# Kernel optimization log

Measured on AMD Instinct MI355X. Metric: run time of the kernel, lower is better.

The kernel has to match this reference:

```python
import jax, jax.numpy as jnp
import numpy as np

B, RES, DIM, H, KD = 16, 32, 768, 12, 64
N = RES * RES          # 1024 tokens
D = KD                 # attn_ratio = 1 -> per-head value dim == key_dim
DH = D * H             # 768
SCALE = KD ** -0.5
LN_EPS = 1e-5


def _bias_idxs():
    # replicate the itertools.product construction: for row-major points,
    # offsets (|dy|,|dx|) are first seen in order dy-major, so id = |dy|*RES + |dx|
    coords = np.arange(N)
    y, x = coords // RES, coords % RES
    dy = np.abs(y[:, None] - y[None, :])
    dx = np.abs(x[:, None] - x[None, :])
    return jnp.asarray(dy * RES + dx, dtype=jnp.int32)  # [N, N]


def setup_inputs() -> dict:
    key = jax.random.key(0)
    ks = jax.random.split(key, 8)
    return {
        "x": jax.random.normal(ks[0], (B, N, DIM), jnp.float32),
        "ln_w": 1.0 + 0.01 * jax.random.normal(ks[1], (DIM,), jnp.float32),
        "ln_b": 0.01 * jax.random.normal(ks[2], (DIM,), jnp.float32),
        "qkv_w": 0.02 * jax.random.normal(ks[3], (3 * H * KD, DIM), jnp.float32),
        "qkv_b": 0.01 * jax.random.normal(ks[4], (3 * H * KD,), jnp.float32),
        "proj_w": 0.02 * jax.random.normal(ks[5], (DIM, DH), jnp.float32),
        "proj_b": 0.01 * jax.random.normal(ks[6], (DIM,), jnp.float32),
        "attn_biases": 0.1 * jax.random.normal(ks[7], (H, RES * RES), jnp.float32),
        "bias_idxs": _bias_idxs(),
    }


def reference(x, ln_w, ln_b, qkv_w, qkv_b, proj_w, proj_b, attn_biases, bias_idxs):
    # LayerNorm over the feature dim
    mu = jnp.mean(x, axis=-1, keepdims=True)
    var = jnp.mean(jnp.square(x - mu), axis=-1, keepdims=True)
    xn = (x - mu) * jax.lax.rsqrt(var + LN_EPS) * ln_w + ln_b

    # fused qkv projection -> [B, N, H, 3*KD], split per head
    qkv = (xn @ qkv_w.T + qkv_b).reshape(B, N, H, 3 * KD)
    q, k, v = jnp.split(qkv, [KD, 2 * KD], axis=3)  # each [B, N, H, KD]

    # gathered relative-position bias: [H, N, N]
    bias = attn_biases[:, bias_idxs]

    # scores + bias -> softmax -> AV
    attn = jnp.einsum("bnhk,bmhk->bhnm", q, k) * SCALE + bias[None]
    attn = jax.nn.softmax(attn, axis=-1)
    out = jnp.einsum("bhnm,bmhd->bnhd", attn, v).reshape(B, N, DH)
    return out @ proj_w.T + proj_b
```

## Files before the change

kernel.cpp:

```cpp
#include <hip/hip_runtime.h>
#include <cstdint>
#include <cstddef>

#define AS1 __attribute__((address_space(1)))
#define AS3 __attribute__((address_space(3)))

typedef float f32x4 __attribute__((ext_vector_type(4)));
typedef __bf16 bf16x8 __attribute__((ext_vector_type(8)));
typedef __bf16 bf16x4 __attribute__((ext_vector_type(4)));
typedef uint32_t u32x4 __attribute__((ext_vector_type(4)));

__device__ __forceinline__ void async_cp16(void* lds, const void* g) {
    __builtin_amdgcn_global_load_lds((AS1 void*)(g), (AS3 void*)(lds), 16, 0, 0);
}

__device__ __forceinline__ bf16x8 frag_of(u32x4 u) {
    return __builtin_bit_cast(bf16x8, u);
}

__global__ __launch_bounds__(256)
void cvt_w(const float* __restrict__ qkvw, const float* __restrict__ projw,
           __bf16* __restrict__ qkvwb, __bf16* __restrict__ projwb) {
    int i = blockIdx.x * 256 + threadIdx.x;
    if (i < 442368) {
        int row = i / 192, c4 = (i - row * 192) * 4;
        int t = (row >= 1536) ? 2 : (row >= 768 ? 1 : 0);
        int rem = row - t * 768;
        int hh = rem >> 6, d = rem & 63;
        int in_row = hh * 192 + t * 64 + d;
        float4 v = *(const float4*)(qkvw + (long)in_row * 768 + c4);
        bf16x4 o;
        o[0] = (__bf16)v.x; o[1] = (__bf16)v.y; o[2] = (__bf16)v.z; o[3] = (__bf16)v.w;
        *(bf16x4*)(qkvwb + (long)row * 768 + c4) = o;
    } else {
        int j = i - 442368;
        float4 v = ((const float4*)projw)[j];
        bf16x4 o;
        o[0] = (__bf16)v.x; o[1] = (__bf16)v.y; o[2] = (__bf16)v.z; o[3] = (__bf16)v.w;
        ((bf16x4*)projwb)[j] = o;
    }
}

__global__ __launch_bounds__(256)
void ln_kernel(const float* __restrict__ x, const float* __restrict__ w,
               const float* __restrict__ bsh, __bf16* __restrict__ xn) {
    const int lane = threadIdx.x & 63;
    const long row = (long)blockIdx.x * 4 + (threadIdx.x >> 6);
    const float4* xr = (const float4*)(x + row * 768);
    float4 v[3];
    v[0] = xr[lane]; v[1] = xr[lane + 64]; v[2] = xr[lane + 128];
    float s = 0.f, ss = 0.f;
#pragma unroll
    for (int i = 0; i < 3; ++i) {
        s  += v[i].x + v[i].y + v[i].z + v[i].w;
        ss += v[i].x * v[i].x + v[i].y * v[i].y + v[i].z * v[i].z + v[i].w * v[i].w;
    }
#pragma unroll
    for (int m = 1; m < 64; m <<= 1) { s += __shfl_xor(s, m); ss += __shfl_xor(ss, m); }
    const float mean = s * (1.f / 768.f);
    const float rstd = rsqrtf(ss * (1.f / 768.f) - mean * mean + 1e-5f);
    const float4* wv = (const float4*)w;
    const float4* bv = (const float4*)bsh;
    bf16x4* outp = (bf16x4*)(xn + row * 768);
#pragma unroll
    for (int i = 0; i < 3; ++i) {
        float4 wi = wv[lane + 64 * i], bi = bv[lane + 64 * i];
        bf16x4 o;
        o[0] = (__bf16)((v[i].x - mean) * rstd * wi.x + bi.x);
        o[1] = (__bf16)((v[i].y - mean) * rstd * wi.y + bi.y);
        o[2] = (__bf16)((v[i].z - mean) * rstd * wi.z + bi.z);
        o[3] = (__bf16)((v[i].w - mean) * rstd * wi.w + bi.w);
        outp[lane + 64 * i] = o;
    }
}

template <int MODE>
__device__ __forceinline__
void gemm_core(char* smem,
               const __bf16* __restrict__ A, const __bf16* __restrict__ Bw,
               const float* __restrict__ bias,
               __bf16* __restrict__ q_out, __bf16* __restrict__ k_out,
               __bf16* __restrict__ vt_out, float* __restrict__ f_out,
               long bm, long bn) {
    constexpr int K = 768;
    const int tid  = threadIdx.x;
    const int lane = tid & 63;
    const int quad = lane >> 4;
    const int l16  = lane & 15;
    const int wave = tid >> 6;
    const int wm = wave >> 1, wn = wave & 1;

    const __bf16* Ab = A  + bm * K;
    const __bf16* Bb = Bw + bn * K;

    const int e0 = tid, e1 = tid + 256;
    const int rA0 = e0 >> 2, c0 = ((e0 & 3) ^ ((e0 >> 3) & 3)) * 8;
    const int rA1 = e1 >> 2, c1 = ((e1 & 3) ^ ((e1 >> 3) & 3)) * 8;
    const int swq = quad ^ ((l16 >> 1) & 3);

    f32x4 acc[4][4] = {};

    auto stage = [&](int t) {
        char* base = smem + (t & 1) * 16384;
        const __bf16* As_ = Ab + t * 32;
        const __bf16* Bs_ = Bb + t * 32;
        async_cp16(base + e0 * 16,        As_ + (long)rA0 * K + c0);
        async_cp16(base + e1 * 16,        As_ + (long)rA1 * K + c1);
        async_cp16(base + 8192 + e0 * 16, Bs_ + (long)rA0 * K + c0);
        async_cp16(base + 8192 + e1 * 16, Bs_ + (long)rA1 * K + c1);
    };

    auto kstep = [&](int buf) {
        const u32x4* Av = (const u32x4*)(smem + buf * 16384);
        const u32x4* Bv = (const u32x4*)(smem + buf * 16384 + 8192);
        bf16x8 af[4], bfr[4];
#pragma unroll
        for (int t = 0; t < 4; ++t) {
            af[t]  = frag_of(Av[(wm * 64 + t * 16 + l16) * 4 + swq]);
            bfr[t] = frag_of(Bv[(wn * 64 + t * 16 + l16) * 4 + swq]);
        }
        __builtin_amdgcn_s_setprio(1);
#pragma unroll
        for (int i = 0; i < 4; ++i)
#pragma unroll
            for (int j = 0; j < 4; ++j) {
                if constexpr (MODE == 0)
                    acc[i][j] = __builtin_amdgcn_mfma_f32_16x16x32_bf16(bfr[j], af[i], acc[i][j], 0, 0, 0);
                else
                    acc[i][j] = __builtin_amdgcn_mfma_f32_16x16x32_bf16(af[i], bfr[j], acc[i][j], 0, 0, 0);
            }
        __builtin_amdgcn_s_setprio(0);
    };

    stage(0); stage(1);
    for (int t = 0; t < 24; ++t) {
        if (t < 23) { asm volatile("s_waitcnt vmcnt(4)" ::: "memory"); }
        else        { asm volatile("s_waitcnt vmcnt(0)" ::: "memory"); }
        __builtin_amdgcn_s_barrier();
        kstep(t & 1);
        asm volatile("s_waitcnt lgkmcnt(0)" ::: "memory");
        __builtin_amdgcn_s_barrier();
        if (t < 22) stage(t + 2);
    }

    if constexpr (MODE == 0) {
#pragma unroll
        for (int j = 0; j < 4; ++j) {
            int col0 = (int)bn + wn * 64 + j * 16 + quad * 4;
            int t  = col0 >= 768;
            int cc = col0 - t * 768;
            int h  = cc >> 6, d = cc & 63;
            int f  = h * 192 + t * 64 + d;
            float4 bb = *(const float4*)(bias + f);
            __bf16* dst = t ? k_out : q_out;
#pragma unroll
            for (int i = 0; i < 4; ++i) {
                long row = bm + wm * 64 + i * 16 + l16;
                long b   = row >> 10;
                long n   = row & 1023;
                bf16x4 pk;
                pk[0] = (__bf16)(acc[i][j][0] + bb.x);
                pk[1] = (__bf16)(acc[i][j][1] + bb.y);
                pk[2] = (__bf16)(acc[i][j][2] + bb.z);
                pk[3] = (__bf16)(acc[i][j][3] + bb.w);
                *(bf16x4*)(dst + ((b * 12 + h) * 1024 + n) * 64 + d) = pk;
            }
        }
    } else if constexpr (MODE == 2) {
#pragma unroll
        for (int j = 0; j < 4; ++j) {
            int cv = (int)bn - 1536 + wn * 64 + j * 16 + l16;
            int h  = cv >> 6, d = cv & 63;
            float bv = bias[h * 192 + 128 + d];
#pragma unroll
            for (int i = 0; i < 4; ++i) {
                long row0 = bm + wm * 64 + i * 16 + quad * 4;
                long b    = row0 >> 10;
                long n0   = row0 & 1023;
                bf16x4 pk;
                pk[0] = (__bf16)(acc[i][j][0] + bv);
                pk[1] = (__bf16)(acc[i][j][1] + bv);
                pk[2] = (__bf16)(acc[i][j][2] + bv);
                pk[3] = (__bf16)(acc[i][j][3] + bv);
                *(bf16x4*)(vt_out + ((b * 12 + h) * 64 + d) * 1024 + n0) = pk;
            }
        }
    } else {
#pragma unroll
        for (int i = 0; i < 4; ++i) {
#pragma unroll
            for (int r = 0; r < 4; ++r) {
                long row = bm + wm * 64 + i * 16 + quad * 4 + r;
#pragma unroll
                for (int j = 0; j < 4; ++j) {
                    int col = (int)bn + wn * 64 + j * 16 + l16;
                    f_out[row * 768 + col] = acc[i][j][r] + bias[col];
                }
            }
        }
    }
}

__global__ __launch_bounds__(256, 4)
void gemm_qkv(const __bf16* __restrict__ A, const __bf16* __restrict__ Bw,
              const float* __restrict__ bias, __bf16* __restrict__ qb,
              __bf16* __restrict__ kb, __bf16* __restrict__ vtb) {
    __shared__ __align__(16) char smem[32768];
    int blk  = blockIdx.x;
    int xcd  = blk & 7;
    int rest = blk >> 3;
    int bx   = rest % 18;
    int byg  = rest / 18;
    long by  = xcd + 8 * byg;
    if (bx < 12)
        gemm_core<0>(smem, A, Bw, bias, qb, kb, nullptr, nullptr, by * 128, (long)bx * 128);
    else
        gemm_core<2>(smem, A, Bw, bias, nullptr, nullptr, vtb, nullptr, by * 128, (long)bx * 128);
}

__global__ __launch_bounds__(256, 4)
void gemm_proj(const __bf16* __restrict__ A, const __bf16* __restrict__ Bw,
               const float* __restrict__ bias, float* __restrict__ out) {
    __shared__ __align__(16) char smem[32768];
    int blk  = blockIdx.x;
    int xcd  = blk & 7;
    int rest = blk >> 3;
    int bx   = rest % 6;
    int byg  = rest / 6;
    long by  = xcd + 8 * byg;
    gemm_core<1>(smem, A, Bw, bias, nullptr, nullptr, nullptr, out,
                 by * 128, (long)bx * 128);
}

__global__ __launch_bounds__(256, 4)
void attn_kernel(const __bf16* __restrict__ Q, const __bf16* __restrict__ Kb,
                 const __bf16* __restrict__ Vt, const float* __restrict__ biases,
                 __bf16* __restrict__ out) {
    __shared__ __align__(16) char smem[28672];
    float* brow = (float*)(smem + 24576);

    const int tid  = threadIdx.x;
    const int lane = tid & 63;
    const int wave = tid >> 6;
    const int quad = lane >> 4;
    const int l16  = lane & 15;
    const int sw   = l16 & 7;
    const int swp  = (l16 >> 1) & 3;

    int blk  = blockIdx.x;
    int xcd  = blk & 7;
    int rest = blk >> 3;
    int qt   = rest & 7;
    int bhg  = rest >> 3;
    int bh_i = xcd + 8 * bhg;
    int b    = bh_i / 12;
    int h    = bh_i - b * 12;

    const long bh = bh_i;
    const __bf16* Qg  = Q  + (bh * 1024 + qt * 128) * 64;
    const __bf16* Kg  = Kb + bh * 1024 * 64;
    const __bf16* Vtg = Vt + bh * 64 * 1024;

    const int rk = tid >> 3;
    const int ck = (tid & 7) ^ (rk & 7);
    const int rv = tid >> 2;
    const int cv = (tid & 3) ^ ((tid >> 3) & 3);

    {
        const float LOG2E = 1.4426950408889634f;
        float4 v = ((const float4*)(biases + (long)h * 1024))[tid];
        float4 o; o.x = v.x * LOG2E; o.y = v.y * LOG2E;
        o.z = v.z * LOG2E; o.w = v.w * LOG2E;
        ((float4*)brow)[tid] = o;
    }
#pragma unroll
    for (int j = 0; j < 4; ++j) {
        int e = tid + 256 * j;
        int r = e >> 3, c = (e & 7) ^ (r & 7);
        async_cp16(smem + e * 16, Qg + r * 64 + c * 8);
    }
    __syncthreads();

    bf16x8 aq[2][2];
    {
        const u32x4* Qv = (const u32x4*)smem;
#pragma unroll
        for (int g = 0; g < 2; ++g) {
            int qrow = wave * 32 + g * 16 + l16;
            aq[g][0] = frag_of(Qv[qrow * 8 + (quad ^ sw)]);
            aq[g][1] = frag_of(Qv[qrow * 8 + ((quad + 4) ^ sw)]);
        }
    }
    __syncthreads();
    async_cp16(smem + tid * 16,        Kg  + rk * 64   + ck * 8);
    async_cp16(smem + 8192 + tid * 16, Vtg + rv * 1024 + cv * 8);
    __syncthreads();

    const int yq = 4 * qt + wave;
    int pdx00[4], pdx01[4], pdx10[4];
#pragma unroll
    for (int r = 0; r < 4; ++r) {
        int d0 = l16 - (quad * 4 + r);
        pdx00[r] = d0 < 0 ? -d0 : d0;
        pdx01[r] = 16 - d0;
        pdx10[r] = 16 + d0;
    }

    const float SSCALE = 0.125f * 1.4426950408889634f;
    float lacc[2] = {0.f, 0.f};
    f32x4 o[2][4] = {};
    char* Pw = smem + 16384 + wave * 2048;
    const int hb = (quad & 1) * 8;
    const int pslotw = (quad >> 1);

    for (int kt = 0; kt < 32; ++kt) {
        const int cb = kt & 1;
        if (kt < 31) {
            const int nb = cb ^ 1;
            async_cp16(smem + nb * 4096 + tid * 16,
                       Kg + (kt + 1) * 2048 + rk * 64 + ck * 8);
            async_cp16(smem + 8192 + nb * 4096 + tid * 16,
                       Vtg + (kt + 1) * 32 + rv * 1024 + cv * 8);
        }

        f32x4 s[2][2];
        const u32x4* Kv = (const u32x4*)(smem + cb * 4096);
#pragma unroll
        for (int nt = 0; nt < 2; ++nt) {
            int krow = nt * 16 + l16;
            bf16x8 k0 = frag_of(Kv[krow * 8 + (quad ^ sw)]);
            bf16x8 k1 = frag_of(Kv[krow * 8 + ((quad + 4) ^ sw)]);
#pragma unroll
            for (int g = 0; g < 2; ++g) {
                f32x4 z = {0.f, 0.f, 0.f, 0.f};
                z = __builtin_amdgcn_mfma_f32_16x16x32_bf16(k0, aq[g][0], z, 0, 0, 0);
                z = __builtin_amdgcn_mfma_f32_16x16x32_bf16(k1, aq[g][1], z, 0, 0, 0);
                s[g][nt] = z;
            }
        }

        int dyv = yq - kt; dyv = dyv < 0 ? -dyv : dyv;
        const float* br = brow + dyv * 32;
#pragma unroll
        for (int g = 0; g < 2; ++g) {
#pragma unroll
            for (int nt = 0; nt < 2; ++nt) {
                const int* pdx = (g == nt) ? pdx00 : (g ? pdx10 : pdx01);
                bf16x4 pk;
#pragma unroll
                for (int r = 0; r < 4; ++r) {
                    float p = __builtin_amdgcn_exp2f(s[g][nt][r] * SSCALE + br[pdx[r]]);
                    lacc[g] += p;
                    pk[r] = (__bf16)p;
                }
                int slot = (nt * 2 + pslotw) ^ swp;
                *(bf16x4*)(Pw + (g * 16 + l16) * 64 + slot * 16 + hb) = pk;
            }
        }

        bf16x8 bp[2];
#pragma unroll
        for (int g = 0; g < 2; ++g)
            bp[g] = frag_of(*(const u32x4*)(Pw + (g * 16 + l16) * 64 + ((quad ^ swp) << 4)));
        const char* Vb = smem + 8192 + cb * 4096;
#pragma unroll
        for (int dt = 0; dt < 4; ++dt) {
            bf16x8 vf = frag_of(*(const u32x4*)(Vb + (dt * 16 + l16) * 64 + ((quad ^ swp) << 4)));
#pragma unroll
            for (int g = 0; g < 2; ++g)
                o[g][dt] = __builtin_amdgcn_mfma_f32_16x16x32_bf16(vf, bp[g], o[g][dt], 0, 0, 0);
        }

        __syncthreads();
    }

#pragma unroll
    for (int g = 0; g < 2; ++g) {
        float la = lacc[g];
        la += __shfl_xor(la, 16);
        la += __shfl_xor(la, 32);
        const float rl = 1.f / la;
        const long n = qt * 128 + wave * 32 + g * 16 + l16;
        __bf16* op = out + ((long)b * 1024 + n) * 768 + h * 64 + quad * 4;
#pragma unroll
        for (int dt = 0; dt < 4; ++dt) {
            bf16x4 ov;
            ov[0] = (__bf16)(o[g][dt][0] * rl);
            ov[1] = (__bf16)(o[g][dt][1] * rl);
            ov[2] = (__bf16)(o[g][dt][2] * rl);
            ov[3] = (__bf16)(o[g][dt][3] * rl);
            *(bf16x4*)(op + dt * 16) = ov;
        }
    }
}

extern "C" void kernel_launch(void* const* d_in, const int* in_sizes, int n_in,
                              void* d_out, int out_size, void* d_ws, size_t ws_size,
                              hipStream_t stream) {
    (void)in_sizes; (void)n_in; (void)out_size; (void)ws_size;
    const float* x      = (const float*)d_in[0];
    const float* ln_w   = (const float*)d_in[1];
    const float* ln_b   = (const float*)d_in[2];
    const float* qkv_w  = (const float*)d_in[3];
    const float* qkv_b  = (const float*)d_in[4];
    const float* proj_w = (const float*)d_in[5];
    const float* proj_b = (const float*)d_in[6];
    const float* ab     = (const float*)d_in[7];
    float* outp = (float*)d_out;

    char* ws = (char*)d_ws;
    __bf16* xn     = (__bf16*)(ws);
    __bf16* aout   = (__bf16*)(ws);
    __bf16* qkvwb  = (__bf16*)(ws + 25165824);
    __bf16* projwb = (__bf16*)(ws + 28704768);
    __bf16* qb     = (__bf16*)(ws + 29884416);
    __bf16* kb     = (__bf16*)(ws + 55050240);
    __bf16* vtb    = (__bf16*)(ws + 80216064);

    cvt_w<<<2304, 256, 0, stream>>>(qkv_w, proj_w, qkvwb, projwb);
    ln_kernel<<<4096, 256, 0, stream>>>(x, ln_w, ln_b, xn);
    gemm_qkv<<<2304, 256, 0, stream>>>(xn, qkvwb, qkv_b, qb, kb, vtb);
    attn_kernel<<<1536, 256, 0, stream>>>(qb, kb, vtb, ab, aout);
    gemm_proj<<<768, 256, 0, stream>>>(aout, projwb, proj_b, outp);
}
```

Baseline: 298.4 us.

## Use 256x256 QKV GEMM tiles with 4-stage pipeline and fuse weight-cast with LayerNorm

The QKV projection moves from 128x128 tiles with 256 threads and double buffering to 256x256 tiles with 512 threads and a four-stage async LDS pipeline. The global-to-LDS copies are interleaved between MFMA phases inside each k-step. This raises data reuse per tile and hides load latency, at the cost of 128 KB of dynamic LDS and fewer, larger blocks (576), which may leave some CUs underused. Separately, the weight-conversion and LayerNorm kernels are merged into a single launch to save one kernel launch.

```diff
diff --git a/kernel.cpp b/kernel.cpp
--- a/kernel.cpp
+++ b/kernel.cpp
@@ -19,33 +19,33 @@
 }
 
 __global__ __launch_bounds__(256)
-void cvt_w(const float* __restrict__ qkvw, const float* __restrict__ projw,
-           __bf16* __restrict__ qkvwb, __bf16* __restrict__ projwb) {
-    int i = blockIdx.x * 256 + threadIdx.x;
-    if (i < 442368) {
-        int row = i / 192, c4 = (i - row * 192) * 4;
-        int t = (row >= 1536) ? 2 : (row >= 768 ? 1 : 0);
-        int rem = row - t * 768;
-        int hh = rem >> 6, d = rem & 63;
-        int in_row = hh * 192 + t * 64 + d;
-        float4 v = *(const float4*)(qkvw + (long)in_row * 768 + c4);
-        bf16x4 o;
-        o[0] = (__bf16)v.x; o[1] = (__bf16)v.y; o[2] = (__bf16)v.z; o[3] = (__bf16)v.w;
-        *(bf16x4*)(qkvwb + (long)row * 768 + c4) = o;
-    } else {
-        int j = i - 442368;
-        float4 v = ((const float4*)projw)[j];
-        bf16x4 o;
-        o[0] = (__bf16)v.x; o[1] = (__bf16)v.y; o[2] = (__bf16)v.z; o[3] = (__bf16)v.w;
-        ((bf16x4*)projwb)[j] = o;
-    }
-}
-
-__global__ __launch_bounds__(256)
-void ln_kernel(const float* __restrict__ x, const float* __restrict__ w,
+void fused_pre(const float* __restrict__ qkvw, const float* __restrict__ projw,
+               __bf16* __restrict__ qkvwb, __bf16* __restrict__ projwb,
+               const float* __restrict__ x, const float* __restrict__ w,
                const float* __restrict__ bsh, __bf16* __restrict__ xn) {
+    if (blockIdx.x < 2304) {
+        int i = blockIdx.x * 256 + threadIdx.x;
+        if (i < 442368) {
+            int row = i / 192, c4 = (i - row * 192) * 4;
+            int t = (row >= 1536) ? 2 : (row >= 768 ? 1 : 0);
+            int rem = row - t * 768;
+            int hh = rem >> 6, d = rem & 63;
+            int in_row = hh * 192 + t * 64 + d;
+            float4 v = *(const float4*)(qkvw + (long)in_row * 768 + c4);
+            bf16x4 o;
+            o[0] = (__bf16)v.x; o[1] = (__bf16)v.y; o[2] = (__bf16)v.z; o[3] = (__bf16)v.w;
+            *(bf16x4*)(qkvwb + (long)row * 768 + c4) = o;
+        } else {
+            int j = i - 442368;
+            float4 v = ((const float4*)projw)[j];
+            bf16x4 o;
+            o[0] = (__bf16)v.x; o[1] = (__bf16)v.y; o[2] = (__bf16)v.z; o[3] = (__bf16)v.w;
+            ((bf16x4*)projwb)[j] = o;
+        }
+        return;
+    }
     const int lane = threadIdx.x & 63;
-    const long row = (long)blockIdx.x * 4 + (threadIdx.x >> 6);
+    const long row = (long)(blockIdx.x - 2304) * 4 + (threadIdx.x >> 6);
     const float4* xr = (const float4*)(x + row * 768);
     float4 v[3];
     v[0] = xr[lane]; v[1] = xr[lane + 64]; v[2] = xr[lane + 128];
@@ -74,14 +74,166 @@
     }
 }
 
-template <int MODE>
+template <int SWAP>
 __device__ __forceinline__
-void gemm_core(char* smem,
-               const __bf16* __restrict__ A, const __bf16* __restrict__ Bw,
-               const float* __restrict__ bias,
-               __bf16* __restrict__ q_out, __bf16* __restrict__ k_out,
-               __bf16* __restrict__ vt_out, float* __restrict__ f_out,
-               long bm, long bn) {
+void gemm256_body(char* smem, const __bf16* __restrict__ A,
+                  const __bf16* __restrict__ Bw, const float* __restrict__ bias,
+                  __bf16* __restrict__ q_out, __bf16* __restrict__ k_out,
+                  __bf16* __restrict__ vt_out, long bm, long bn) {
+    const int tid  = threadIdx.x;
+    const int lane = tid & 63;
+    const int quad = lane >> 4;
+    const int l16  = lane & 15;
+    const int wave = tid >> 6;
+    const int wm = wave >> 2, wn = wave & 3;
+
+    const __bf16* Ag = A  + bm * 768;
+    const __bf16* Bg = Bw + bn * 768;
+    const int r0  = tid >> 2;
+    const int sc  = ((tid & 3) ^ ((tid >> 3) & 3)) * 8;
+    const int swq = quad ^ ((l16 >> 1) & 3);
+
+    f32x4 acc[8][4] = {};
+
+    auto stage = [&](int t) {
+        char* base = smem + (size_t)(t & 3) * 32768;
+        const __bf16* As_ = Ag + t * 32 + sc;
+        const __bf16* Bs_ = Bg + t * 32 + sc;
+        async_cp16(base + tid * 16,                 As_ + (size_t)r0 * 768);
+        async_cp16(base + (tid + 512) * 16,         As_ + (size_t)(r0 + 128) * 768);
+        async_cp16(base + 16384 + tid * 16,         Bs_ + (size_t)r0 * 768);
+        async_cp16(base + 16384 + (tid + 512) * 16, Bs_ + (size_t)(r0 + 128) * 768);
+    };
+
+#define MFMA8(MLO, NLO)                                                        \
+    __builtin_amdgcn_s_setprio(1);                                             \
+    _Pragma("unroll") for (int mi = 0; mi < 4; ++mi)                           \
+    _Pragma("unroll") for (int ni = 0; ni < 2; ++ni) {                         \
+        int m = (MLO) + mi, n = (NLO) + ni;                                    \
+        if constexpr (SWAP)                                                    \
+            acc[m][n] = __builtin_amdgcn_mfma_f32_16x16x32_bf16(bfv[n & 3], af[mi], acc[m][n], 0, 0, 0); \
+        else                                                                   \
+            acc[m][n] = __builtin_amdgcn_mfma_f32_16x16x32_bf16(af[mi], bfv[n & 3], acc[m][n], 0, 0, 0); \
+    }                                                                          \
+    __builtin_amdgcn_s_setprio(0);
+
+    auto tile_phases = [&](int buf, int stg, bool do_stage) {
+        const u32x4* Ab2 = (const u32x4*)(smem + (size_t)buf * 32768);
+        const u32x4* Bb2 = (const u32x4*)(smem + (size_t)buf * 32768 + 16384);
+        char* sb = smem + (size_t)(stg & 3) * 32768;
+        const __bf16* As_ = Ag + stg * 32 + sc;
+        const __bf16* Bs_ = Bg + stg * 32 + sc;
+        bf16x8 af[4], bfv[4];
+#pragma unroll
+        for (int m = 0; m < 4; ++m)
+            af[m] = frag_of(Ab2[(wm * 128 + m * 16 + l16) * 4 + swq]);
+#pragma unroll
+        for (int n = 0; n < 2; ++n)
+            bfv[n] = frag_of(Bb2[(wn * 64 + n * 16 + l16) * 4 + swq]);
+        if (do_stage) async_cp16(sb + tid * 16, As_ + (size_t)r0 * 768);
+        MFMA8(0, 0)
+        __builtin_amdgcn_s_barrier();
+#pragma unroll
+        for (int n = 2; n < 4; ++n)
+            bfv[n] = frag_of(Bb2[(wn * 64 + n * 16 + l16) * 4 + swq]);
+        if (do_stage) async_cp16(sb + (tid + 512) * 16, As_ + (size_t)(r0 + 128) * 768);
+        MFMA8(0, 2)
+        __builtin_amdgcn_s_barrier();
+#pragma unroll
+        for (int m = 0; m < 4; ++m)
+            af[m] = frag_of(Ab2[(wm * 128 + (m + 4) * 16 + l16) * 4 + swq]);
+        if (do_stage) async_cp16(sb + 16384 + tid * 16, Bs_ + (size_t)r0 * 768);
+        MFMA8(4, 2)
+        __builtin_amdgcn_s_barrier();
+        if (do_stage) async_cp16(sb + 16384 + (tid + 512) * 16, Bs_ + (size_t)(r0 + 128) * 768);
+        MFMA8(4, 0)
+    };
+#undef MFMA8
+
+    stage(0); stage(1); stage(2);
+    for (int t = 0; t < 21; ++t) {
+        asm volatile("s_waitcnt vmcnt(8)" ::: "memory");
+        __builtin_amdgcn_s_barrier();
+        tile_phases(t & 3, t + 3, true);
+    }
+    asm volatile("s_waitcnt vmcnt(8)" ::: "memory");
+    __builtin_amdgcn_s_barrier();
+    tile_phases(1, 0, false);
+    asm volatile("s_waitcnt vmcnt(4)" ::: "memory");
+    __builtin_amdgcn_s_barrier();
+    tile_phases(2, 0, false);
+    asm volatile("s_waitcnt vmcnt(0)" ::: "memory");
+    __builtin_amdgcn_s_barrier();
+    tile_phases(3, 0, false);
+
+    if constexpr (SWAP) {
+#pragma unroll
+        for (int n = 0; n < 4; ++n) {
+            int col0 = (int)bn + wn * 64 + n * 16 + quad * 4;
+            int t_ = col0 >= 768;
+            int cc = col0 - t_ * 768;
+            int hh = cc >> 6, dd = cc & 63;
+            int f  = hh * 192 + t_ * 64 + dd;
+            float4 bb = *(const float4*)(bias + f);
+            __bf16* dst = t_ ? k_out : q_out;
+#pragma unroll
+            for (int m = 0; m < 8; ++m) {
+                long row = bm + wm * 128 + m * 16 + l16;
+                long b   = row >> 10;
+                long nn  = row & 1023;
+                bf16x4 pk;
+                pk[0] = (__bf16)(acc[m][n][0] + bb.x);
+                pk[1] = (__bf16)(acc[m][n][1] + bb.y);
+                pk[2] = (__bf16)(acc[m][n][2] + bb.z);
+                pk[3] = (__bf16)(acc[m][n][3] + bb.w);
+                *(bf16x4*)(dst + ((b * 12 + hh) * 1024 + nn) * 64 + dd) = pk;
+            }
+        }
+    } else {
+#pragma unroll
+        for (int n = 0; n < 4; ++n) {
+            int cv = (int)bn - 1536 + wn * 64 + n * 16 + l16;
+            int hh = cv >> 6, dd = cv & 63;
+            float bv = bias[hh * 192 + 128 + dd];
+#pragma unroll
+            for (int m = 0; m < 8; ++m) {
+                long row0 = bm + wm * 128 + m * 16 + quad * 4;
+                long b    = row0 >> 10;
+                long n0   = row0 & 1023;
+                bf16x4 pk;
+                pk[0] = (__bf16)(acc[m][n][0] + bv);
+                pk[1] = (__bf16)(acc[m][n][1] + bv);
+                pk[2] = (__bf16)(acc[m][n][2] + bv);
+                pk[3] = (__bf16)(acc[m][n][3] + bv);
+                *(bf16x4*)(vt_out + ((b * 12 + hh) * 64 + dd) * 1024 + n0) = pk;
+            }
+        }
+    }
+}
+
+__global__ __launch_bounds__(512, 2)
+void gemm_qkv(const __bf16* __restrict__ A, const __bf16* __restrict__ Bw,
+              const float* __restrict__ bias, __bf16* __restrict__ qb,
+              __bf16* __restrict__ kb, __bf16* __restrict__ vtb) {
+    extern __shared__ char smem[];
+    int blk  = blockIdx.x;
+    int xcd  = blk & 7;
+    int rest = blk >> 3;
+    int bx   = rest % 9;
+    int byg  = rest / 9;
+    long by  = xcd + 8 * byg;
+    long bm  = by * 256, bn = (long)bx * 256;
+    if (bx < 6)
+        gemm256_body<1>(smem, A, Bw, bias, qb, kb, nullptr, bm, bn);
+    else
+        gemm256_body<0>(smem, A, Bw, bias, nullptr, nullptr, vtb, bm, bn);
+}
+
+__device__ __forceinline__
+void gemm_core1(char* smem,
+                const __bf16* __restrict__ A, const __bf16* __restrict__ Bw,
+                const float* __restrict__ bias, float* __restrict__ f_out,
+                long bm, long bn) {
     constexpr int K = 768;
     const int tid  = threadIdx.x;
     const int lane = tid & 63;
@@ -123,12 +275,8 @@
 #pragma unroll
         for (int i = 0; i < 4; ++i)
 #pragma unroll
-            for (int j = 0; j < 4; ++j) {
-                if constexpr (MODE == 0)
-                    acc[i][j] = __builtin_amdgcn_mfma_f32_16x16x32_bf16(bfr[j], af[i], acc[i][j], 0, 0, 0);
-                else
-                    acc[i][j] = __builtin_amdgcn_mfma_f32_16x16x32_bf16(af[i], bfr[j], acc[i][j], 0, 0, 0);
-            }
+            for (int j = 0; j < 4; ++j)
+                acc[i][j] = __builtin_amdgcn_mfma_f32_16x16x32_bf16(af[i], bfr[j], acc[i][j], 0, 0, 0);
         __builtin_amdgcn_s_setprio(0);
     };
 
@@ -143,79 +291,18 @@
         if (t < 22) stage(t + 2);
     }
 
-    if constexpr (MODE == 0) {
-#pragma unroll
-        for (int j = 0; j < 4; ++j) {
-            int col0 = (int)bn + wn * 64 + j * 16 + quad * 4;
-            int t  = col0 >= 768;
-            int cc = col0 - t * 768;
-            int h  = cc >> 6, d = cc & 63;
-            int f  = h * 192 + t * 64 + d;
-            float4 bb = *(const float4*)(bias + f);
-            __bf16* dst = t ? k_out : q_out;
-#pragma unroll
-            for (int i = 0; i < 4; ++i) {
-                long row = bm + wm * 64 + i * 16 + l16;
-                long b   = row >> 10;
-                long n   = row & 1023;
-                bf16x4 pk;
-                pk[0] = (__bf16)(acc[i][j][0] + bb.x);
-                pk[1] = (__bf16)(acc[i][j][1] + bb.y);
-                pk[2] = (__bf16)(acc[i][j][2] + bb.z);
-                pk[3] = (__bf16)(acc[i][j][3] + bb.w);
-                *(bf16x4*)(dst + ((b * 12 + h) * 1024 + n) * 64 + d) = pk;
+#pragma unroll
+    for (int i = 0; i < 4; ++i) {
+#pragma unroll
+        for (int r = 0; r < 4; ++r) {
+            long row = bm + wm * 64 + i * 16 + quad * 4 + r;
+#pragma unroll
+            for (int j = 0; j < 4; ++j) {
+                int col = (int)bn + wn * 64 + j * 16 + l16;
+                f_out[row * 768 + col] = acc[i][j][r] + bias[col];
             }
         }
-    } else if constexpr (MODE == 2) {
-#pragma unroll
-        for (int j = 0; j < 4; ++j) {
-            int cv = (int)bn - 1536 + wn * 64 + j * 16 + l16;
-            int h  = cv >> 6, d = cv & 63;
-            float bv = bias[h * 192 + 128 + d];
-#pragma unroll
-            for (int i = 0; i < 4; ++i) {
-                long row0 = bm + wm * 64 + i * 16 + quad * 4;
-                long b    = row0 >> 10;
-                long n0   = row0 & 1023;
-                bf16x4 pk;
-                pk[0] = (__bf16)(acc[i][j][0] + bv);
-                pk[1] = (__bf16)(acc[i][j][1] + bv);
-                pk[2] = (__bf16)(acc[i][j][2] + bv);
-                pk[3] = (__bf16)(acc[i][j][3] + bv);
-                *(bf16x4*)(vt_out + ((b * 12 + h) * 64 + d) * 1024 + n0) = pk;
-            }
-        }
-    } else {
-#pragma unroll
-        for (int i = 0; i < 4; ++i) {
-#pragma unroll
-            for (int r = 0; r < 4; ++r) {
-                long row = bm + wm * 64 + i * 16 + quad * 4 + r;
-#pragma unroll
-                for (int j = 0; j < 4; ++j) {
-                    int col = (int)bn + wn * 64 + j * 16 + l16;
-                    f_out[row * 768 + col] = acc[i][j][r] + bias[col];
-                }
-            }
-        }
-    }
-}
-
-__global__ __launch_bounds__(256, 4)
-void gemm_qkv(const __bf16* __restrict__ A, const __bf16* __restrict__ Bw,
-              const float* __restrict__ bias, __bf16* __restrict__ qb,
-              __bf16* __restrict__ kb, __bf16* __restrict__ vtb) {
-    __shared__ __align__(16) char smem[32768];
-    int blk  = blockIdx.x;
-    int xcd  = blk & 7;
-    int rest = blk >> 3;
-    int bx   = rest % 18;
-    int byg  = rest / 18;
-    long by  = xcd + 8 * byg;
-    if (bx < 12)
-        gemm_core<0>(smem, A, Bw, bias, qb, kb, nullptr, nullptr, by * 128, (long)bx * 128);
-    else
-        gemm_core<2>(smem, A, Bw, bias, nullptr, nullptr, vtb, nullptr, by * 128, (long)bx * 128);
+    }
 }
 
 __global__ __launch_bounds__(256, 4)
@@ -228,8 +315,7 @@
     int bx   = rest % 6;
     int byg  = rest / 6;
     long by  = xcd + 8 * byg;
-    gemm_core<1>(smem, A, Bw, bias, nullptr, nullptr, nullptr, out,
-                 by * 128, (long)bx * 128);
+    gemm_core1(smem, A, Bw, bias, out, by * 128, (long)bx * 128);
 }
 
 __global__ __launch_bounds__(256, 4)
@@ -417,9 +503,9 @@
     __bf16* kb     = (__bf16*)(ws + 55050240);
     __bf16* vtb    = (__bf16*)(ws + 80216064);
 
-    cvt_w<<<2304, 256, 0, stream>>>(qkv_w, proj_w, qkvwb, projwb);
-    ln_kernel<<<4096, 256, 0, stream>>>(x, ln_w, ln_b, xn);
-    gemm_qkv<<<2304, 256, 0, stream>>>(xn, qkvwb, qkv_b, qb, kb, vtb);
+    fused_pre<<<6400, 256, 0, stream>>>(qkv_w, proj_w, qkvwb, projwb,
+                                        x, ln_w, ln_b, xn);
+    gemm_qkv<<<576, 512, 131072, stream>>>(xn, qkvwb, qkv_b, qb, kb, vtb);
     attn_kernel<<<1536, 256, 0, stream>>>(qb, kb, vtb, ab, aout);
     gemm_proj<<<768, 256, 0, stream>>>(aout, projwb, proj_b, outp);
 }
```

New measurement: 311.0 us. 1.04x slower.
